# Kernel tuning notes

Hardware: AMD Instinct MI355X
Metric: run time of the kernel (lower is better)

## Reference

```python
import jax, jax.numpy as jnp
import numpy as np

VOCAB = 32000
EMBED = 512
NUM_CLASS = 5
LEAVES = 8192
N_NODES = 2 * LEAVES - 1


def _build_tree(n_leaves):
    """Balanced binary tree over n_leaves leaves, nodes listed in post-order
    (children always appear before their parent), matching the recursive
    traversal order of the original torch module."""
    is_leaf, word, left, right = [], [], [], []

    def rec(lo, hi):
        if hi - lo == 1:
            is_leaf.append(1)
            word.append((lo * 2654435761) % VOCAB)
            left.append(0)
            right.append(0)
        else:
            mid = (lo + hi) // 2
            l = rec(lo, mid)
            r = rec(mid, hi)
            is_leaf.append(0)
            word.append(0)
            left.append(l)
            right.append(r)
        return len(is_leaf) - 1

    rec(0, n_leaves)
    return (np.asarray(is_leaf, np.int32), np.asarray(word, np.int32),
            np.asarray(left, np.int32), np.asarray(right, np.int32))


def setup_inputs() -> dict:
    key = jax.random.key(0)
    k1, k2, k3, k4, k5 = jax.random.split(key, 5)
    is_leaf, word, left, right = _build_tree(LEAVES)
    scale = 0.05
    return {
        "is_leaf": jnp.asarray(is_leaf),
        "word": jnp.asarray(word),
        "left": jnp.asarray(left),
        "right": jnp.asarray(right),
        "emb": jax.random.normal(k1, (VOCAB, EMBED), jnp.float32) * scale,
        "W": jax.random.normal(k2, (EMBED, 2 * EMBED), jnp.float32) * scale,
        "bW": jax.random.normal(k3, (EMBED,), jnp.float32) * scale,
        "P": jax.random.normal(k4, (NUM_CLASS, EMBED), jnp.float32) * scale,
        "bP": jax.random.normal(k5, (NUM_CLASS,), jnp.float32) * scale,
    }


def reference(is_leaf, word, left, right, emb, W, bW, P, bP):
    n = is_leaf.shape[0]

    def step(H, xs):
        idx, lf, wd, li, ri = xs
        # internal node: relu(W @ [h_left; h_right] + b)
        pair = jnp.concatenate([H[li], H[ri]])          # [2D]
        internal = pair @ W.T + bW                       # [D]
        leaf = emb[wd]                                   # [D]
        h = jax.nn.relu(jnp.where(lf == 1, leaf, internal))
        return H.at[idx].set(h), None

    H0 = jnp.zeros((n, EMBED), emb.dtype)
    xs = (jnp.arange(n, dtype=jnp.int32), is_leaf, word, left, right)
    H, _ = jax.lax.scan(step, H0, xs)
    # per-node class logits, rows in traversal (post-)order: [N, num_class]
    return H @ P.T + bP
```

## Files before the change

kernel.cpp:

```cpp
#include <hip/hip_runtime.h>


#define EMBED 512
#define K2    1024
#define WOFF  (EMBED * K2)

typedef _Float16 half8 __attribute__((ext_vector_type(8)));
typedef float    floatx4 __attribute__((ext_vector_type(4)));

__device__ __forceinline__ float relu_f(float x) { return fmaxf(x, 0.0f); }

#define GLDS16(gp, lp)                                                        \
    __builtin_amdgcn_global_load_lds(                                         \
        (const __attribute__((address_space(1))) void*)(gp),                  \
        (__attribute__((address_space(3))) void*)(lp), 16, 0, 0)

#define MFMA16(a, b, c) __builtin_amdgcn_mfma_f32_16x16x32_f16(a, b, c, 0, 0, 0)

__global__ __launch_bounds__(256)
void packleaf(const float* __restrict__ W, const float* __restrict__ emb,
              const int* __restrict__ word,
              _Float16* __restrict__ Whp,
              _Float16* __restrict__ Hh, _Float16* __restrict__ Hl,
              int nLeaves)
{
    int tid = threadIdx.x;
    int wave = tid >> 6, lane = tid & 63;

    {
        int t = blockIdx.x * 256 + tid;
        int n = t >> 7, kc = t & 127;
        const float* src = W + (size_t)n * K2 + kc * 8;
        int s = kc >> 2, quad = kc & 3;
        int ln = (quad << 4) | (n & 15);
        size_t off = (size_t)(n >> 4) * 16384 + (size_t)s * 512 + (size_t)ln * 8;
        half8 hi, lo;
#pragma unroll
        for (int j = 0; j < 8; ++j) {
            float w = src[j];
            _Float16 h16 = (_Float16)w;
            hi[j] = h16;
            lo[j] = (_Float16)(w - (float)h16);
        }
        *(half8*)(Whp + off) = hi;
        *(half8*)(Whp + WOFF + off) = lo;
    }
    {
#pragma unroll
        for (int i = 0; i < 8; ++i) {
            int m = blockIdx.x * 32 + wave * 8 + i;
            if (m < nLeaves) {
                int wd = word[2 * m - __popc(m)];
                const float4* src = (const float4*)(emb + (size_t)wd * EMBED) + lane * 2;
                float4 a = src[0], b = src[1];
                float v[8] = {a.x, a.y, a.z, a.w, b.x, b.y, b.z, b.w};
                half8 hi, lo;
#pragma unroll
                for (int j = 0; j < 8; ++j) {
                    float x = relu_f(v[j]);
                    _Float16 h16 = (_Float16)x;
                    hi[j] = h16;
                    lo[j] = (_Float16)(x - (float)h16);
                }
                *(half8*)(Hh + (size_t)m * EMBED + lane * 8) = hi;
                *(half8*)(Hl + (size_t)m * EMBED + lane * 8) = lo;
            }
        }
    }
}

__global__ __launch_bounds__(256)
void gemm_lvl(const _Float16* __restrict__ Ap,
              const _Float16* __restrict__ Wp,
              const float* __restrict__ bW,
              _Float16* __restrict__ Cp,
              int hoff)
{
    __shared__ _Float16 As[16384];
    __shared__ float Red[4096];

    int tid = threadIdx.x;
    int wave = tid >> 6, lane = tid & 63;
    int q = lane >> 4, r = lane & 15;
    int slice = wave >> 1, nh = wave & 1;
    int bm0 = blockIdx.x * 64, bn0 = blockIdx.y * 64;

    const _Float16* Asrc = Ap + (size_t)(nh ? hoff : 0)
                         + (size_t)(bm0 + r) * 1024 + slice * 512 + q * 8;

    floatx4 acc[4][2];
#pragma unroll
    for (int t = 0; t < 4; ++t)
#pragma unroll
        for (int u = 0; u < 2; ++u) acc[t][u] = (floatx4){0.f, 0.f, 0.f, 0.f};

    for (int kc = 0; kc < 8; ++kc) {
#pragma unroll
        for (int t = 0; t < 4; ++t)
#pragma unroll
            for (int s2 = 0; s2 < 2; ++s2) {
                const _Float16* gp = Asrc + t * (16 * 1024) + kc * 64 + s2 * 32;
                GLDS16(gp, &As[(slice * 16 + t * 4 + s2 * 2 + nh) * 512]);
            }
        __syncthreads();

#pragma unroll
        for (int s2 = 0; s2 < 2; ++s2) {
            half8 bh[2], bl[2];
#pragma unroll
            for (int u = 0; u < 2; ++u) {
                const _Float16* pb = Wp + (size_t)(blockIdx.y * 4 + nh * 2 + u) * 16384
                                   + (size_t)(slice * 16 + kc * 2 + s2) * 512 + lane * 8;
                bh[u] = *(const half8*)pb;
                bl[u] = *(const half8*)(pb + WOFF);
            }
#pragma unroll
            for (int t = 0; t < 4; ++t) {
                half8 ah = *(const half8*)&As[(slice * 16 + t * 4 + s2 * 2 + 0) * 512 + lane * 8];
                half8 al = *(const half8*)&As[(slice * 16 + t * 4 + s2 * 2 + 1) * 512 + lane * 8];
#pragma unroll
                for (int u = 0; u < 2; ++u) {
                    acc[t][u] = MFMA16(ah, bh[u], acc[t][u]);
                    acc[t][u] = MFMA16(ah, bl[u], acc[t][u]);
                    acc[t][u] = MFMA16(al, bh[u], acc[t][u]);
                }
            }
        }
        __syncthreads();
    }

    if (slice == 1) {
#pragma unroll
        for (int t = 0; t < 4; ++t)
#pragma unroll
            for (int u = 0; u < 2; ++u)
#pragma unroll
                for (int reg = 0; reg < 4; ++reg)
                    Red[(t * 16 + q * 4 + reg) * 64 + nh * 32 + u * 16 + r]
                        = acc[t][u][reg];
    }
    __syncthreads();
    if (slice == 0) {
#pragma unroll
        for (int t = 0; t < 4; ++t)
#pragma unroll
            for (int u = 0; u < 2; ++u) {
                int col = bn0 + nh * 32 + u * 16 + r;
                float bw = bW[col];
#pragma unroll
                for (int reg = 0; reg < 4; ++reg) {
                    int ml = t * 16 + q * 4 + reg;
                    float v = acc[t][u][reg]
                            + Red[ml * 64 + nh * 32 + u * 16 + r];
                    float x = relu_f(v + bw);
                    _Float16 hi = (_Float16)x;
                    size_t o = (size_t)(bm0 + ml) * EMBED + col;
                    Cp[o] = hi;
                    Cp[o + hoff] = (_Float16)(x - (float)hi);
                }
            }
    }
}

__global__ __launch_bounds__(256)
void gemm_splitk32(const _Float16* __restrict__ Ap, const _Float16* __restrict__ Wp,
                   const float* __restrict__ bW,
                   _Float16* __restrict__ Cp, int hoff)
{
    __shared__ float red[4096];

    int tid = threadIdx.x;
    int wave = tid >> 6, lane = tid & 63;
    int q = lane >> 4, r = lane & 15;
    int m0 = blockIdx.x * 32, n0 = blockIdx.y * 32;

    const _Float16 *pAh[2], *pAl[2];
#pragma unroll
    for (int mi = 0; mi < 2; ++mi) {
        int m = m0 + mi * 16 + r;
        int prow = 2 * m + (wave >> 1);
        int kb = (wave & 1) * 256;
        pAh[mi] = Ap + (size_t)prow * EMBED + kb + q * 8;
        pAl[mi] = pAh[mi] + hoff;
    }
    const _Float16* pB[2];
#pragma unroll
    for (int u = 0; u < 2; ++u)
        pB[u] = Wp + (size_t)(blockIdx.y * 2 + u) * 16384
              + (size_t)(wave * 8) * 512 + lane * 8;

    floatx4 acc[2][2];
#pragma unroll
    for (int mi = 0; mi < 2; ++mi)
#pragma unroll
        for (int u = 0; u < 2; ++u) acc[mi][u] = (floatx4){0.f, 0.f, 0.f, 0.f};

#pragma unroll
    for (int s = 0; s < 8; ++s) {
        half8 ah[2], al[2], bh[2], bl[2];
#pragma unroll
        for (int mi = 0; mi < 2; ++mi) {
            ah[mi] = *(const half8*)(pAh[mi] + s * 32);
            al[mi] = *(const half8*)(pAl[mi] + s * 32);
        }
#pragma unroll
        for (int u = 0; u < 2; ++u) {
            bh[u] = *(const half8*)(pB[u] + s * 512);
            bl[u] = *(const half8*)(pB[u] + s * 512 + WOFF);
        }
#pragma unroll
        for (int mi = 0; mi < 2; ++mi)
#pragma unroll
            for (int u = 0; u < 2; ++u) {
                acc[mi][u] = MFMA16(ah[mi], bh[u], acc[mi][u]);
                acc[mi][u] = MFMA16(ah[mi], bl[u], acc[mi][u]);
                acc[mi][u] = MFMA16(al[mi], bh[u], acc[mi][u]);
            }
    }

#pragma unroll
    for (int mi = 0; mi < 2; ++mi)
#pragma unroll
        for (int u = 0; u < 2; ++u)
#pragma unroll
            for (int reg = 0; reg < 4; ++reg)
                red[wave * 1024 + (mi * 16 + q * 4 + reg) * 32 + u * 16 + r]
                    = acc[mi][u][reg];
    __syncthreads();

    int row = tid >> 3, c4 = (tid & 7) * 4;
    _Float16 hi4[4], lo4[4];
#pragma unroll
    for (int j = 0; j < 4; ++j) {
        int c = row * 32 + c4 + j;
        float v = red[c] + red[1024 + c] + red[2048 + c] + red[3072 + c];
        float x = relu_f(v + bW[n0 + c4 + j]);
        _Float16 hi = (_Float16)x;
        hi4[j] = hi;
        lo4[j] = (_Float16)(x - (float)hi);
    }
    size_t o = (size_t)(m0 + row) * EMBED + n0 + c4;
#pragma unroll
    for (int j = 0; j < 4; ++j) { Cp[o + j] = hi4[j]; Cp[o + hoff + j] = lo4[j]; }
}

__global__ __launch_bounds__(256)
void gemm_splitk(const _Float16* __restrict__ Ap, const _Float16* __restrict__ Wp,
                 const float* __restrict__ bW,
                 _Float16* __restrict__ Cp, int hoff, int M)
{
    __shared__ float red[1024];

    int tid = threadIdx.x;
    int wave = tid >> 6, lane = tid & 63;
    int q = lane >> 4, r = lane & 15;
    int mt = blockIdx.x, u = blockIdx.y;

    int m = mt * 16 + r;
    if (m >= M) m = M - 1;
    int prow = 2 * m + (wave >> 1);
    int kb = (wave & 1) * 256;
    const _Float16* pAh = Ap + (size_t)prow * EMBED + kb + q * 8;
    const _Float16* pAl = pAh + hoff;
    const _Float16* pB  = Wp + (size_t)u * 16384 + (size_t)(wave * 8) * 512 + lane * 8;

    floatx4 acc = (floatx4){0.f, 0.f, 0.f, 0.f};
#pragma unroll
    for (int s = 0; s < 8; ++s) {
        half8 ah = *(const half8*)(pAh + s * 32);
        half8 al = *(const half8*)(pAl + s * 32);
        half8 bh = *(const half8*)(pB + s * 512);
        half8 bl = *(const half8*)(pB + s * 512 + WOFF);
        acc = MFMA16(ah, bh, acc);
        acc = MFMA16(ah, bl, acc);
        acc = MFMA16(al, bh, acc);
    }
#pragma unroll
    for (int reg = 0; reg < 4; ++reg)
        red[wave * 256 + (q * 4 + reg) * 16 + r] = acc[reg];
    __syncthreads();

    int row = tid >> 4, col = tid & 15;
    float v = red[row * 16 + col] + red[256 + row * 16 + col]
            + red[512 + row * 16 + col] + red[768 + row * 16 + col];
    int mm = mt * 16 + row;
    if (mm < M) {
        int colg = u * 16 + col;
        float x = relu_f(v + bW[colg]);
        _Float16 hi = (_Float16)x;
        size_t o = (size_t)mm * EMBED + colg;
        Cp[o] = hi;
        Cp[o + hoff] = (_Float16)(x - (float)hi);
    }
}

__global__ __launch_bounds__(256)
void out_kernel(const _Float16* __restrict__ Hh, const _Float16* __restrict__ Hl,
                const float* __restrict__ P, const float* __restrict__ bP,
                float* __restrict__ out, int nNodes)
{
    int t = blockIdx.x * 256 + threadIdx.x;
    int j = t >> 6, lane = t & 63;
    if (j >= nNodes) return;
    int v = nNodes - j;
    int h = 13 - (31 - __clz(v));
    int m = j - ((nNodes + 1) - (1 << (13 - h + 1)));
    int node = ((m + 1) << (h + 1)) - 2 - __popc(m);

    half8 hv = *(const half8*)(Hh + (size_t)j * EMBED + lane * 8);
    half8 lv = *(const half8*)(Hl + (size_t)j * EMBED + lane * 8);
    float hx[8];
#pragma unroll
    for (int k = 0; k < 8; ++k) hx[k] = (float)hv[k] + (float)lv[k];
    float s[5];
#pragma unroll
    for (int c = 0; c < 5; ++c) {
        const float* p = P + c * EMBED + lane * 8;
        float4 p0 = *(const float4*)p;
        float4 p1 = *(const float4*)(p + 4);
        s[c] = hx[0] * p0.x + hx[1] * p0.y + hx[2] * p0.z + hx[3] * p0.w
             + hx[4] * p1.x + hx[5] * p1.y + hx[6] * p1.z + hx[7] * p1.w;
    }
#pragma unroll
    for (int o = 32; o > 0; o >>= 1)
#pragma unroll
        for (int c = 0; c < 5; ++c)
            s[c] += __shfl_down(s[c], o, 64);
    if (lane == 0) {
#pragma unroll
        for (int c = 0; c < 5; ++c)
            out[(size_t)node * 5 + c] = s[c] + bP[c];
    }
}

extern "C" void kernel_launch(void* const* d_in, const int* in_sizes, int n_in,
                              void* d_out, int out_size, void* d_ws, size_t ws_size,
                              hipStream_t stream)
{
    const int*   word = (const int*)d_in[1];
    const float* emb  = (const float*)d_in[4];
    const float* W    = (const float*)d_in[5];
    const float* bW   = (const float*)d_in[6];
    const float* P    = (const float*)d_in[7];
    const float* bP   = (const float*)d_in[8];
    float* out = (float*)d_out;

    int nNodes  = in_sizes[0];
    int nLeaves = (nNodes + 1) / 2;
    int nRows   = nNodes + 1;

    int hoff = nRows * EMBED;
    _Float16* Hh  = (_Float16*)d_ws;
    _Float16* Hl  = Hh + hoff;
    _Float16* Whp = Hl + hoff;

    auto roff = [&](int h) { return nRows - (1 << (14 - h)); };

    packleaf<<<dim3(256), dim3(256), 0, stream>>>(
        W, emb, word, Whp, Hh, Hl, nLeaves);

    for (int h = 1; h <= 2; ++h) {
        int M = 1 << (13 - h);
        gemm_lvl<<<dim3(M / 64, 8), dim3(256), 0, stream>>>(
            Hh + (size_t)roff(h - 1) * EMBED, Whp, bW,
            Hh + (size_t)roff(h) * EMBED, hoff);
    }
    for (int h = 3; h <= 4; ++h) {
        int M = 1 << (13 - h);
        gemm_splitk32<<<dim3(M / 32, 16), dim3(256), 0, stream>>>(
            Hh + (size_t)roff(h - 1) * EMBED, Whp, bW,
            Hh + (size_t)roff(h) * EMBED, hoff);
    }
    for (int h = 5; h <= 13; ++h) {
        int M = 1 << (13 - h);
        gemm_splitk<<<dim3((M + 15) / 16, 32), dim3(256), 0, stream>>>(
            Hh + (size_t)roff(h - 1) * EMBED, Whp, bW,
            Hh + (size_t)roff(h) * EMBED, hoff, M);
    }
    out_kernel<<<dim3((nNodes * 64 + 255) / 256), dim3(256), 0, stream>>>(
        Hh, Hl, P, bP, out, nNodes);
}
```

Baseline: 236.2 us.

## Fuse pairs of upper tree levels into one launch with redundant recompute

Tree levels 5 through 12 are processed in pairs by one kernel. Some blocks compute level h as before. The extra blocks recompute their 32 rows of level h in full (all 512 columns) into shared memory and then produce level h+1 from there. This halves the number of serial launches for the small top levels, which are bound by launch and latency cost. The price is duplicated level-h work in every recompute block, plus heavy per-block weight reads and register pressure from the 16 accumulator tiles.

```diff
diff --git a/kernel.cpp b/kernel.cpp
--- a/kernel.cpp
+++ b/kernel.cpp
@@ -4,6 +4,7 @@
 #define EMBED 512
 #define K2    1024
 #define WOFF  (EMBED * K2)
+#define HSTR  520
 
 typedef _Float16 half8 __attribute__((ext_vector_type(8)));
 typedef float    floatx4 __attribute__((ext_vector_type(4)));
@@ -295,6 +296,143 @@
 }
 
 __global__ __launch_bounds__(256)
+void fused_pair(const _Float16* __restrict__ Pp,
+                const _Float16* __restrict__ Wp,
+                const float* __restrict__ bW,
+                _Float16* __restrict__ Ch, _Float16* __restrict__ Cn,
+                int hoff, int Mh, int Mn, int mtiles_h)
+{
+    __shared__ _Float16 Hs[2][32 * HSTR];
+    __shared__ float red[1024];
+
+    int tid = threadIdx.x;
+    int wave = tid >> 6, lane = tid & 63;
+    int q = lane >> 4, r = lane & 15;
+    int u = blockIdx.y;
+
+    if ((int)blockIdx.x < mtiles_h) {
+        int mt = blockIdx.x;
+        int m = mt * 16 + r;
+        if (m >= Mh) m = Mh - 1;
+        int prow = 2 * m + (wave >> 1);
+        int kb = (wave & 1) * 256;
+        const _Float16* pAh = Pp + (size_t)prow * EMBED + kb + q * 8;
+        const _Float16* pAl = pAh + hoff;
+        const _Float16* pB  = Wp + (size_t)u * 16384 + (size_t)(wave * 8) * 512 + lane * 8;
+
+        floatx4 acc = (floatx4){0.f, 0.f, 0.f, 0.f};
+#pragma unroll
+        for (int s = 0; s < 8; ++s) {
+            half8 ah = *(const half8*)(pAh + s * 32);
+            half8 al = *(const half8*)(pAl + s * 32);
+            half8 bh = *(const half8*)(pB + s * 512);
+            half8 bl = *(const half8*)(pB + s * 512 + WOFF);
+            acc = MFMA16(ah, bh, acc);
+            acc = MFMA16(ah, bl, acc);
+            acc = MFMA16(al, bh, acc);
+        }
+#pragma unroll
+        for (int reg = 0; reg < 4; ++reg)
+            red[wave * 256 + (q * 4 + reg) * 16 + r] = acc[reg];
+        __syncthreads();
+
+        int row = tid >> 4, col = tid & 15;
+        float v = red[row * 16 + col] + red[256 + row * 16 + col]
+                + red[512 + row * 16 + col] + red[768 + row * 16 + col];
+        int mm = mt * 16 + row;
+        if (mm < Mh) {
+            int colg = u * 16 + col;
+            float x = relu_f(v + bW[colg]);
+            _Float16 hi = (_Float16)x;
+            size_t o = (size_t)mm * EMBED + colg;
+            Ch[o] = hi;
+            Ch[o + hoff] = (_Float16)(x - (float)hi);
+        }
+        return;
+    }
+
+    int mt2 = blockIdx.x - mtiles_h;
+
+    {
+        int a = wave >> 1, chh = wave & 1;
+        int rowh = mt2 * 32 + a * 16 + r;
+        if (rowh >= Mh) rowh = Mh - 1;
+
+        floatx4 acc[16];
+#pragma unroll
+        for (int j = 0; j < 16; ++j) acc[j] = (floatx4){0.f, 0.f, 0.f, 0.f};
+
+        for (int s = 0; s < 32; ++s) {
+            const _Float16* pa = Pp + (size_t)(2 * rowh + (s >> 4)) * EMBED
+                               + (s & 15) * 32 + q * 8;
+            half8 ah = *(const half8*)pa;
+            half8 al = *(const half8*)(pa + hoff);
+#pragma unroll
+            for (int j = 0; j < 16; ++j) {
+                const _Float16* pb = Wp + (size_t)(chh * 16 + j) * 16384
+                                   + (size_t)s * 512 + lane * 8;
+                half8 bh = *(const half8*)pb;
+                half8 bl = *(const half8*)(pb + WOFF);
+                acc[j] = MFMA16(ah, bh, acc[j]);
+                acc[j] = MFMA16(ah, bl, acc[j]);
+                acc[j] = MFMA16(al, bh, acc[j]);
+            }
+        }
+#pragma unroll
+        for (int j = 0; j < 16; ++j) {
+            int col = (chh * 16 + j) * 16 + r;
+            float bw = bW[col];
+#pragma unroll
+            for (int reg = 0; reg < 4; ++reg) {
+                int lrow = a * 16 + q * 4 + reg;
+                float x = relu_f(acc[j][reg] + bw);
+                _Float16 hi = (_Float16)x;
+                Hs[0][lrow * HSTR + col] = hi;
+                Hs[1][lrow * HSTR + col] = (_Float16)(x - (float)hi);
+            }
+        }
+    }
+    __syncthreads();
+
+    {
+        int rl = r;
+        if (rl >= Mn) rl = Mn - 1;
+        int lrow = 2 * rl + (wave >> 1);
+        int kb = (wave & 1) * 256;
+        const _Float16* pB = Wp + (size_t)u * 16384 + (size_t)(wave * 8) * 512 + lane * 8;
+
+        floatx4 acc = (floatx4){0.f, 0.f, 0.f, 0.f};
+#pragma unroll
+        for (int s = 0; s < 8; ++s) {
+            half8 ah = *(const half8*)&Hs[0][lrow * HSTR + kb + s * 32 + q * 8];
+            half8 al = *(const half8*)&Hs[1][lrow * HSTR + kb + s * 32 + q * 8];
+            half8 bh = *(const half8*)(pB + s * 512);
+            half8 bl = *(const half8*)(pB + s * 512 + WOFF);
+            acc = MFMA16(ah, bh, acc);
+            acc = MFMA16(ah, bl, acc);
+            acc = MFMA16(al, bh, acc);
+        }
+#pragma unroll
+        for (int reg = 0; reg < 4; ++reg)
+            red[wave * 256 + (q * 4 + reg) * 16 + r] = acc[reg];
+        __syncthreads();
+
+        int row = tid >> 4, col = tid & 15;
+        float v = red[row * 16 + col] + red[256 + row * 16 + col]
+                + red[512 + row * 16 + col] + red[768 + row * 16 + col];
+        int mm = mt2 * 16 + row;
+        if (mm < Mn) {
+            int colg = u * 16 + col;
+            float x = relu_f(v + bW[colg]);
+            _Float16 hi = (_Float16)x;
+            size_t o = (size_t)mm * EMBED + colg;
+            Cn[o] = hi;
+            Cn[o + hoff] = (_Float16)(x - (float)hi);
+        }
+    }
+}
+
+__global__ __launch_bounds__(256)
 void out_kernel(const _Float16* __restrict__ Hh, const _Float16* __restrict__ Hl,
                 const float* __restrict__ P, const float* __restrict__ bP,
                 float* __restrict__ out, int nNodes)
@@ -355,6 +493,7 @@
     _Float16* Whp = Hl + hoff;
 
     auto roff = [&](int h) { return nRows - (1 << (14 - h)); };
+    auto lvl  = [&](int h) { return Hh + (size_t)roff(h) * EMBED; };
 
     packleaf<<<dim3(256), dim3(256), 0, stream>>>(
         W, emb, word, Whp, Hh, Hl, nLeaves);
@@ -362,21 +501,24 @@
     for (int h = 1; h <= 2; ++h) {
         int M = 1 << (13 - h);
         gemm_lvl<<<dim3(M / 64, 8), dim3(256), 0, stream>>>(
-            Hh + (size_t)roff(h - 1) * EMBED, Whp, bW,
-            Hh + (size_t)roff(h) * EMBED, hoff);
+            lvl(h - 1), Whp, bW, lvl(h), hoff);
     }
     for (int h = 3; h <= 4; ++h) {
         int M = 1 << (13 - h);
         gemm_splitk32<<<dim3(M / 32, 16), dim3(256), 0, stream>>>(
-            Hh + (size_t)roff(h - 1) * EMBED, Whp, bW,
-            Hh + (size_t)roff(h) * EMBED, hoff);
-    }
-    for (int h = 5; h <= 13; ++h) {
-        int M = 1 << (13 - h);
-        gemm_splitk<<<dim3((M + 15) / 16, 32), dim3(256), 0, stream>>>(
-            Hh + (size_t)roff(h - 1) * EMBED, Whp, bW,
-            Hh + (size_t)roff(h) * EMBED, hoff, M);
-    }
+            lvl(h - 1), Whp, bW, lvl(h), hoff);
+    }
+    for (int h = 5; h <= 11; h += 2) {
+        int Mh = 1 << (13 - h);
+        int Mn = Mh >> 1;
+        int mt_h = (Mh + 15) / 16;
+        int mt_n = (Mn + 15) / 16;
+        fused_pair<<<dim3(mt_h + mt_n, 32), dim3(256), 0, stream>>>(
+            lvl(h - 1), Whp, bW, lvl(h), lvl(h + 1), hoff, Mh, Mn, mt_h);
+    }
+    gemm_splitk<<<dim3(1, 32), dim3(256), 0, stream>>>(
+        lvl(12), Whp, bW, lvl(13), hoff, 1);
+
     out_kernel<<<dim3((nNodes * 64 + 255) / 256), dim3(256), 0, stream>>>(
         Hh, Hl, P, bP, out, nNodes);
 }
```

New measurement: 490.9 us. 108% more time.
